# Kernel optimization log

Hardware: AMD Instinct MI355X
Metric: run time of the kernel (lower is better)

## Reference

```python
import jax, jax.numpy as jnp
import numpy as np

TEMPERATURE = 1.0


def setup_inputs() -> dict:
    key = jax.random.key(0)
    kq, kk, kv = jax.random.split(key, 3)
    shape = (2, 16, 2048, 64)  # B, H, L, D
    q = jax.random.normal(kq, shape, dtype=jnp.float32)
    k = jax.random.normal(kk, shape, dtype=jnp.float32)
    v = jax.random.normal(kv, shape, dtype=jnp.float32)
    return {"q": q, "k": k, "v": v}


def reference(q, k, v):
    # q, k, v: [B, H, L, D]
    L = q.shape[2]
    # scores: [B, H, L, L]; note: divided by temperature, NOT sqrt(D), per source
    scores = jnp.einsum("bhqd,bhkd->bhqk", q, k) / TEMPERATURE
    # causal mask: position j > i masked with -inf
    causal = jnp.tril(jnp.ones((L, L), dtype=bool))  # True = keep
    scores = jnp.where(causal, scores, -jnp.inf)
    attn = jax.nn.softmax(scores, axis=-1)
    out = jnp.einsum("bhqk,bhkd->bhqd", attn, v)
    return out
```

## Files before the change

### kernel.cpp

```cpp
#include <hip/hip_runtime.h>
#include <math.h>


typedef __attribute__((ext_vector_type(8))) _Float16 f16x8;
typedef __attribute__((ext_vector_type(4))) _Float16 f16x4;
typedef __attribute__((ext_vector_type(4))) float f32x4;
typedef __attribute__((ext_vector_type(16))) float f32x16;
typedef unsigned short u16;
typedef unsigned int u32;
typedef __attribute__((ext_vector_type(8))) u16 u16x8;
typedef __attribute__((ext_vector_type(4))) u32 u32x4;

constexpr int Lq = 2048;
constexpr int Dd = 64;
constexpr int KT = 64;
constexpr int BH = 32;
constexpr float LOG2E = 1.44269504088896f;

#define SWZB(row, bcol) ((((row) * 128) + (bcol)) ^ (((row) & 7) << 4))

#define GLOAD_LDS16(g, l)                                                     \
  __builtin_amdgcn_global_load_lds(                                           \
      (const __attribute__((address_space(1))) void*)(g),                     \
      (__attribute__((address_space(3))) void*)(l), 16, 0, 0)

static __device__ __forceinline__ u16 f2h(float x) {
  return __builtin_bit_cast(u16, (_Float16)x);
}

static __device__ __forceinline__ float tmax16(const f32x16& v) {
  float a = fmaxf(v[0], v[1]), b = fmaxf(v[2], v[3]);
  float c = fmaxf(v[4], v[5]), d = fmaxf(v[6], v[7]);
  float e = fmaxf(v[8], v[9]), f = fmaxf(v[10], v[11]);
  float g = fmaxf(v[12], v[13]), h = fmaxf(v[14], v[15]);
  a = fmaxf(a, b); c = fmaxf(c, d); e = fmaxf(e, f); g = fmaxf(g, h);
  return fmaxf(fmaxf(a, c), fmaxf(e, g));
}
static __device__ __forceinline__ float tsum16(const f32x16& v) {
  float a = v[0] + v[1], b = v[2] + v[3], c = v[4] + v[5], d = v[6] + v[7];
  float e = v[8] + v[9], f = v[10] + v[11], g = v[12] + v[13], h = v[14] + v[15];
  a += b; c += d; e += f; g += h;
  return (a + c) + (e + g);
}

constexpr int PREP_KB = (BH * Lq * Dd) / (256 * 16);

__global__ __launch_bounds__(256)
void attn_prep(const float* __restrict__ K, const float* __restrict__ V,
               u16* __restrict__ Kh, u16* __restrict__ VTh) {
  const int b = blockIdx.x;
  const int tid = threadIdx.x;
  if (b < PREP_KB) {
    const size_t base = ((size_t)b * 256 + tid) * 16;
    const f32x4* src = reinterpret_cast<const f32x4*>(K + base);
    u16x8 o0, o1;
    #pragma unroll
    for (int i = 0; i < 2; ++i) {
      const f32x4 a = src[i];
      #pragma unroll
      for (int j = 0; j < 4; ++j) o0[i * 4 + j] = f2h(a[j]);
    }
    #pragma unroll
    for (int i = 0; i < 2; ++i) {
      const f32x4 a = src[2 + i];
      #pragma unroll
      for (int j = 0; j < 4; ++j) o1[i * 4 + j] = f2h(a[j]);
    }
    *reinterpret_cast<u16x8*>(Kh + base) = o0;
    *reinterpret_cast<u16x8*>(Kh + base + 8) = o1;
  } else {
    __shared__ u16 lt[64][66];
    const int vb = b - PREP_KB;
    const int h = vb >> 5, tt = vb & 31;
    const float* Vt = V + ((size_t)h * Lq + tt * 64) * Dd;
    const int r = tid & 63, dg = tid >> 6;
    #pragma unroll
    for (int i = 0; i < 4; ++i) {
      const f32x4 a = *reinterpret_cast<const f32x4*>(Vt + (size_t)r * Dd + dg * 16 + i * 4);
      #pragma unroll
      for (int j = 0; j < 2; ++j) {
        const unsigned two =
            (unsigned)f2h(a[2 * j]) | ((unsigned)f2h(a[2 * j + 1]) << 16);
        *reinterpret_cast<unsigned*>(&lt[r][dg * 16 + i * 4 + j * 2]) = two;
      }
    }
    __syncthreads();
    const int d = tid >> 2, kq = tid & 3;
    u16x8 w0, w1;
    #pragma unroll
    for (int j = 0; j < 8; ++j) w0[j] = lt[kq * 16 + j][d];
    #pragma unroll
    for (int j = 0; j < 8; ++j) w1[j] = lt[kq * 16 + 8 + j][d];
    u16* dst = VTh + ((size_t)h * Dd + d) * Lq + tt * 64 + kq * 16;
    *reinterpret_cast<u16x8*>(dst) = w0;
    *reinterpret_cast<u16x8*>(dst + 8) = w1;
  }
}

__global__ __launch_bounds__(128)
void attn_main(const float* __restrict__ Q, float* __restrict__ O,
               const u16* __restrict__ Kh, const u16* __restrict__ VTh) {
  __shared__ char ks[2][8192];
  __shared__ char vt2[2][8192];
  __shared__ float bc[2][32];

  const int tid  = threadIdx.x;
  const int lane = tid & 63;
  const int wv   = tid >> 6;
  const int l31  = lane & 31;
  const int hi   = lane >> 5;

  const int b = blockIdx.x;
  const int chunk = 31 - (b >> 5);
  const int h = b & 31;

  const float* Qb = Q + (size_t)h * Lq * Dd;
  float*       Ob = O + (size_t)h * Lq * Dd;
  const u16*   Kb = Kh + (size_t)h * Lq * Dd;
  const u16*   Vb = VTh + (size_t)h * Dd * Lq;

  const int T    = chunk + 1;
  const int qrow = chunk * 64 + wv * 32;

  f16x8 qf[4];
  #pragma unroll
  for (int kc = 0; kc < 4; ++kc) {
    const float* qp = Qb + (size_t)(qrow + l31) * Dd + kc * 16 + hi * 8;
    const f32x4 a = *reinterpret_cast<const f32x4*>(qp);
    const f32x4 c = *reinterpret_cast<const f32x4*>(qp + 4);
    f16x8 q8;
    #pragma unroll
    for (int e = 0; e < 4; ++e) {
      q8[e]     = (_Float16)(a[e] * LOG2E);
      q8[e + 4] = (_Float16)(c[e] * LOG2E);
    }
    qf[kc] = q8;
  }

  float m = -INFINITY, lsum = 0.f;
  f32x16 o0, o1;
  #pragma unroll
  for (int e = 0; e < 16; ++e) { o0[e] = 0.f; o1[e] = 0.f; }

  const int rr = lane >> 3;
  const int c0 = (lane & 7) ^ rr;

  #pragma unroll
  for (int it = 0; it < 4; ++it) {
    const int row = wv * 32 + it * 8 + rr;
    GLOAD_LDS16(Kb + (size_t)row * Dd + c0 * 8,
                &ks[0][wv * 4096 + it * 1024 + lane * 16]);
    GLOAD_LDS16(Vb + (size_t)row * Lq + c0 * 8,
                &vt2[0][wv * 4096 + it * 1024 + lane * 16]);
  }

  int cur = 0;
  #pragma unroll 1
  for (int t = 0; t < T; ++t) {
    __syncthreads();
    if (t + 1 < T) {
      #pragma unroll
      for (int it = 0; it < 4; ++it) {
        const int row = wv * 32 + it * 8 + rr;
        GLOAD_LDS16(Kb + (size_t)((t + 1) * KT + row) * Dd + c0 * 8,
                    &ks[cur ^ 1][wv * 4096 + it * 1024 + lane * 16]);
        GLOAD_LDS16(Vb + (size_t)row * Lq + (t + 1) * KT + c0 * 8,
                    &vt2[cur ^ 1][wv * 4096 + it * 1024 + lane * 16]);
      }
    }
    const char* kb = ks[cur];
    const char* vb = vt2[cur];
    const bool last  = (t == T - 1);
    const bool have1 = !(last && wv == 0);

    f32x16 st0, st1;
    #pragma unroll
    for (int e = 0; e < 16; ++e) { st0[e] = 0.f; st1[e] = 0.f; }
    __builtin_amdgcn_s_setprio(1);
    #pragma unroll
    for (int kc = 0; kc < 4; ++kc) {
      const f16x8 kf = *reinterpret_cast<const f16x8*>(
          kb + SWZB(l31, kc * 32 + hi * 16));
      st0 = __builtin_amdgcn_mfma_f32_32x32x16_f16(kf, qf[kc], st0, 0, 0, 0);
    }
    if (have1) {
      #pragma unroll
      for (int kc = 0; kc < 4; ++kc) {
        const f16x8 kf = *reinterpret_cast<const f16x8*>(
            kb + SWZB(32 + l31, kc * 32 + hi * 16));
        st1 = __builtin_amdgcn_mfma_f32_32x32x16_f16(kf, qf[kc], st1, 0, 0, 0);
      }
    }
    __builtin_amdgcn_s_setprio(0);

    if (last) {
      #pragma unroll
      for (int r = 0; r < 16; ++r) {
        const int crow = (r & 3) + 8 * (r >> 2) + 4 * hi;
        if (wv == 0) { if (crow > l31) st0[r] = -INFINITY; }
        else         { if (crow > l31) st1[r] = -INFINITY; }
      }
    }

    float pm = tmax16(st0);
    if (have1) pm = fmaxf(pm, tmax16(st1));
    pm = fmaxf(pm, __shfl_xor(pm, 32));

    if (__any(pm > m + 8.f * LOG2E)) {
      const float mn = fmaxf(m, pm);
      const float sc = exp2f(m - mn);
      m = mn;
      lsum *= sc;
      if (hi == 0) bc[wv][l31] = sc;
      const f32x4 s0 = *reinterpret_cast<const f32x4*>(&bc[wv][4 * hi]);
      const f32x4 s1 = *reinterpret_cast<const f32x4*>(&bc[wv][8 + 4 * hi]);
      const f32x4 s2 = *reinterpret_cast<const f32x4*>(&bc[wv][16 + 4 * hi]);
      const f32x4 s3 = *reinterpret_cast<const f32x4*>(&bc[wv][24 + 4 * hi]);
      #pragma unroll
      for (int r = 0; r < 16; ++r) {
        const float fac = (r < 4) ? s0[r & 3] : (r < 8) ? s1[r & 3]
                        : (r < 12) ? s2[r & 3] : s3[r & 3];
        o0[r] *= fac;
        o1[r] *= fac;
      }
    }

    #pragma unroll
    for (int r = 0; r < 16; ++r) st0[r] = exp2f(st0[r] - m);
    float rs = tsum16(st0);
    if (have1) {
      #pragma unroll
      for (int r = 0; r < 16; ++r) st1[r] = exp2f(st1[r] - m);
      rs += tsum16(st1);
    }
    rs += __shfl_xor(rs, 32);
    lsum += rs;

    #pragma unroll
    for (int ksub = 0; ksub < 2; ++ksub) {
      if (ksub == 1 && !have1) break;
      const f32x16& st = (ksub == 0) ? st0 : st1;
      #pragma unroll
      for (int ks2 = 0; ks2 < 2; ++ks2) {
        const u32 pe0 = __builtin_bit_cast(u32,
            __builtin_amdgcn_cvt_pkrtz(st[8 * ks2 + 0], st[8 * ks2 + 1]));
        const u32 pe1 = __builtin_bit_cast(u32,
            __builtin_amdgcn_cvt_pkrtz(st[8 * ks2 + 2], st[8 * ks2 + 3]));
        const u32 po0 = __builtin_bit_cast(u32,
            __builtin_amdgcn_cvt_pkrtz(st[8 * ks2 + 4], st[8 * ks2 + 5]));
        const u32 po1 = __builtin_bit_cast(u32,
            __builtin_amdgcn_cvt_pkrtz(st[8 * ks2 + 6], st[8 * ks2 + 7]));
        const u32 ss0 = __shfl_xor(hi ? pe0 : po0, 32);
        const u32 ss1 = __shfl_xor(hi ? pe1 : po1, 32);
        u32x4 w;
        w[0] = hi ? ss0 : pe0;
        w[1] = hi ? ss1 : pe1;
        w[2] = hi ? po0 : ss0;
        w[3] = hi ? po1 : ss1;
        const f16x8 pa = __builtin_bit_cast(f16x8, w);
        const int cb = ksub * 64 + ks2 * 32 + hi * 16;
        const f16x8 v0 = *reinterpret_cast<const f16x8*>(vb + SWZB(l31, cb));
        const f16x8 v1 = *reinterpret_cast<const f16x8*>(vb + SWZB(32 + l31, cb));
        __builtin_amdgcn_s_setprio(1);
        o0 = __builtin_amdgcn_mfma_f32_32x32x16_f16(pa, v0, o0, 0, 0, 0);
        o1 = __builtin_amdgcn_mfma_f32_32x32x16_f16(pa, v1, o1, 0, 0, 0);
        __builtin_amdgcn_s_setprio(0);
      }
    }
    cur ^= 1;
  }

  const float inv = 1.f / lsum;
  if (hi == 0) bc[wv][l31] = inv;
  const f32x4 i0 = *reinterpret_cast<const f32x4*>(&bc[wv][4 * hi]);
  const f32x4 i1 = *reinterpret_cast<const f32x4*>(&bc[wv][8 + 4 * hi]);
  const f32x4 i2 = *reinterpret_cast<const f32x4*>(&bc[wv][16 + 4 * hi]);
  const f32x4 i3 = *reinterpret_cast<const f32x4*>(&bc[wv][24 + 4 * hi]);
  #pragma unroll
  for (int r = 0; r < 16; ++r) {
    const int crow = (r & 3) + 8 * (r >> 2) + 4 * hi;
    const float fac = (r < 4) ? i0[r & 3] : (r < 8) ? i1[r & 3]
                    : (r < 12) ? i2[r & 3] : i3[r & 3];
    float* op = Ob + (size_t)(qrow + crow) * Dd + l31;
    op[0]  = o0[r] * fac;
    op[32] = o1[r] * fac;
  }
}

__global__ __launch_bounds__(256)
void causal_attn_fb(const float* __restrict__ Q, const float* __restrict__ K,
                    const float* __restrict__ V, float* __restrict__ O) {
  __shared__ char ks[2][KT * 128];
  __shared__ char vt[2][Dd * 128];
  __shared__ char pl[4][16 * 128];
  const int tid = threadIdx.x, lane = tid & 63, wv = tid >> 6;
  const int l15 = lane & 15, g = lane >> 4;
  const int kg = tid & 15, dq = tid >> 4;
  const int bh = blockIdx.x / 16, pr = blockIdx.x % 16;
  const size_t base = (size_t)bh * Lq * Dd;
  const float* Qb = Q + base; const float* Kb = K + base;
  const float* Vb = V + base; float* Ob = O + base;
  char* pw = pl[wv];
  #pragma unroll 1
  for (int phase = 0; phase < 2; ++phase) {
    const int chunk = (phase == 0) ? pr : (31 - pr);
    const int row0 = chunk * 64, T = chunk + 1, qrow = row0 + wv * 16;
    f16x8 qf[2];
    #pragma unroll
    for (int kk = 0; kk < 2; ++kk) {
      const float* qp = Qb + (size_t)(qrow + l15) * Dd + kk * 32 + g * 8;
      const f32x4 a = *reinterpret_cast<const f32x4*>(qp);
      const f32x4 b = *reinterpret_cast<const f32x4*>(qp + 4);
      f16x8 q8;
      #pragma unroll
      for (int i = 0; i < 4; ++i) { q8[i] = (_Float16)a[i]; q8[i+4] = (_Float16)b[i]; }
      qf[kk] = q8;
    }
    float m[4], lsum[4]; f32x4 o[4];
    #pragma unroll
    for (int r = 0; r < 4; ++r) { m[r] = -INFINITY; lsum[r] = 0.f; }
    #pragma unroll
    for (int nd = 0; nd < 4; ++nd) o[nd] = f32x4{0.f, 0.f, 0.f, 0.f};
    {
      f32x4 kreg[4], vreg[4];
      #pragma unroll
      for (int i = 0; i < 4; ++i) {
        const int c = tid + i * 256;
        kreg[i] = *reinterpret_cast<const f32x4*>(Kb + (size_t)(c >> 4) * Dd + (c & 15) * 4);
      }
      #pragma unroll
      for (int c = 0; c < 4; ++c)
        vreg[c] = *reinterpret_cast<const f32x4*>(Vb + (size_t)(kg * 4 + c) * Dd + dq * 4);
      __syncthreads();
      #pragma unroll
      for (int i = 0; i < 4; ++i) {
        const int c = tid + i * 256;
        f16x4 hh;
        #pragma unroll
        for (int jj = 0; jj < 4; ++jj) hh[jj] = (_Float16)kreg[i][jj];
        *reinterpret_cast<f16x4*>(ks[0] + SWZB(c >> 4, (c & 15) * 8)) = hh;
      }
      #pragma unroll
      for (int jj = 0; jj < 4; ++jj) {
        f16x4 hh;
        #pragma unroll
        for (int c = 0; c < 4; ++c) hh[c] = (_Float16)vreg[c][jj];
        *reinterpret_cast<f16x4*>(vt[0] + SWZB(dq * 4 + jj, kg * 8)) = hh;
      }
    }
    int cur = 0;
    #pragma unroll 1
    for (int t = 0; t < T; ++t) {
      __syncthreads();
      const char* kb = ks[cur]; const char* vb = vt[cur];
      f32x4 kreg[4], vreg[4];
      const bool pfn = (t + 1 < T);
      if (pfn) {
        const float* Kt = Kb + (size_t)(t + 1) * KT * Dd;
        const float* Vt = Vb + (size_t)(t + 1) * KT * Dd;
        #pragma unroll
        for (int i = 0; i < 4; ++i) {
          const int c = tid + i * 256;
          kreg[i] = *reinterpret_cast<const f32x4*>(Kt + (size_t)(c >> 4) * Dd + (c & 15) * 4);
        }
        #pragma unroll
        for (int c = 0; c < 4; ++c)
          vreg[c] = *reinterpret_cast<const f32x4*>(Vt + (size_t)(kg * 4 + c) * Dd + dq * 4);
      }
      f32x4 s[4];
      #pragma unroll
      for (int n = 0; n < 4; ++n) s[n] = f32x4{0.f, 0.f, 0.f, 0.f};
      #pragma unroll
      for (int kk = 0; kk < 2; ++kk) {
        #pragma unroll
        for (int n = 0; n < 4; ++n) {
          const f16x8 kf = *reinterpret_cast<const f16x8*>(kb + SWZB(n * 16 + l15, kk * 64 + g * 16));
          s[n] = __builtin_amdgcn_mfma_f32_16x16x32_f16(qf[kk], kf, s[n], 0, 0, 0);
        }
      }
      if (t == T - 1) {
        #pragma unroll
        for (int n = 0; n < 4; ++n) {
          const int key = t * KT + n * 16 + l15;
          #pragma unroll
          for (int r = 0; r < 4; ++r)
            if (key > qrow + 4 * g + r) s[n][r] = -INFINITY;
        }
      }
      float rmax[4], rsum[4], scale[4];
      #pragma unroll
      for (int r = 0; r < 4; ++r)
        rmax[r] = fmaxf(fmaxf(s[0][r], s[1][r]), fmaxf(s[2][r], s[3][r]));
      #pragma unroll
      for (int mk = 1; mk <= 8; mk <<= 1) {
        #pragma unroll
        for (int r = 0; r < 4; ++r) rmax[r] = fmaxf(rmax[r], __shfl_xor(rmax[r], mk));
      }
      #pragma unroll
      for (int r = 0; r < 4; ++r) {
        const float mn = fmaxf(m[r], rmax[r]);
        scale[r] = __expf(m[r] - mn); m[r] = mn;
      }
      #pragma unroll
      for (int n = 0; n < 4; ++n) {
        #pragma unroll
        for (int r = 0; r < 4; ++r) s[n][r] = __expf(s[n][r] - m[r]);
      }
      #pragma unroll
      for (int r = 0; r < 4; ++r) rsum[r] = (s[0][r] + s[1][r]) + (s[2][r] + s[3][r]);
      #pragma unroll
      for (int mk = 1; mk <= 8; mk <<= 1) {
        #pragma unroll
        for (int r = 0; r < 4; ++r) rsum[r] += __shfl_xor(rsum[r], mk);
      }
      #pragma unroll
      for (int r = 0; r < 4; ++r) lsum[r] = lsum[r] * scale[r] + rsum[r];
      #pragma unroll
      for (int nd = 0; nd < 4; ++nd) {
        #pragma unroll
        for (int r = 0; r < 4; ++r) o[nd][r] *= scale[r];
      }
      #pragma unroll
      for (int n = 0; n < 4; ++n) {
        #pragma unroll
        for (int r = 0; r < 4; ++r)
          *reinterpret_cast<_Float16*>(pw + SWZB(4 * g + r, (n * 16 + l15) * 2)) = (_Float16)s[n][r];
      }
      asm volatile("s_waitcnt lgkmcnt(0)" ::: "memory");
      __builtin_amdgcn_sched_barrier(0);
      #pragma unroll
      for (int kblk = 0; kblk < 2; ++kblk) {
        const f16x8 pf = *reinterpret_cast<const f16x8*>(pw + SWZB(l15, kblk * 64 + g * 16));
        #pragma unroll
        for (int nd = 0; nd < 4; ++nd) {
          const f16x8 vf = *reinterpret_cast<const f16x8*>(vb + SWZB(nd * 16 + l15, kblk * 64 + g * 16));
          o[nd] = __builtin_amdgcn_mfma_f32_16x16x32_f16(pf, vf, o[nd], 0, 0, 0);
        }
      }
      if (pfn) {
        char* kn = ks[cur ^ 1]; char* vn = vt[cur ^ 1];
        #pragma unroll
        for (int i = 0; i < 4; ++i) {
          const int c = tid + i * 256;
          f16x4 hh;
          #pragma unroll
          for (int jj = 0; jj < 4; ++jj) hh[jj] = (_Float16)kreg[i][jj];
          *reinterpret_cast<f16x4*>(kn + SWZB(c >> 4, (c & 15) * 8)) = hh;
        }
        #pragma unroll
        for (int jj = 0; jj < 4; ++jj) {
          f16x4 hh;
          #pragma unroll
          for (int c = 0; c < 4; ++c) hh[c] = (_Float16)vreg[c][jj];
          *reinterpret_cast<f16x4*>(vn + SWZB(dq * 4 + jj, kg * 8)) = hh;
        }
      }
      cur ^= 1;
    }
    float inv[4];
    #pragma unroll
    for (int r = 0; r < 4; ++r) inv[r] = 1.f / lsum[r];
    #pragma unroll
    for (int nd = 0; nd < 4; ++nd) {
      #pragma unroll
      for (int r = 0; r < 4; ++r)
        Ob[(size_t)(qrow + 4 * g + r) * Dd + nd * 16 + l15] = o[nd][r] * inv[r];
    }
  }
}

extern "C" void kernel_launch(void* const* d_in, const int* in_sizes, int n_in,
                              void* d_out, int out_size, void* d_ws, size_t ws_size,
                              hipStream_t stream) {
  const float* q = (const float*)d_in[0];
  const float* k = (const float*)d_in[1];
  const float* v = (const float*)d_in[2];
  float* o = (float*)d_out;
  const size_t elems = (size_t)BH * Lq * Dd;
  const size_t need = elems * 2 * 2;
  if (ws_size >= need) {
    u16* Kh = (u16*)d_ws;
    u16* VTh = Kh + elems;
    attn_prep<<<dim3(2 * PREP_KB), dim3(256), 0, stream>>>(k, v, Kh, VTh);
    attn_main<<<dim3(BH * 32), dim3(128), 0, stream>>>(q, o, Kh, VTh);
  } else {
    causal_attn_fb<<<dim3(BH * 16), dim3(256), 0, stream>>>(q, k, v, o);
  }
  (void)in_sizes; (void)n_in; (void)out_size;
}
```

Before: 84.43 us.

## Use single-wave blocks with 32-row query and key tiles, dropping block barriers

Each attention block now has one 64-lane wave and handles 32 query rows, with 32-key tiles, launching twice as many blocks. Because the block is a single wave, __syncthreads is replaced by explicit vmcnt waits on the async global-to-LDS prefetches. V tiles use a new 64-byte-row swizzle. This aims for finer-grained causal load balance, more resident blocks and no cross-wave barriers, at the cost of twice the loop iterations per row, more per-tile overhead and each block reloading K/V independently, which doubles K/V traffic.

```diff
diff --git a/kernel.cpp b/kernel.cpp
--- a/kernel.cpp
+++ b/kernel.cpp
@@ -18,6 +18,7 @@
 constexpr float LOG2E = 1.44269504088896f;
 
 #define SWZB(row, bcol) ((((row) * 128) + (bcol)) ^ (((row) & 7) << 4))
+#define SWZB64(row, bcol) ((((row) * 64) + (bcol)) ^ ((((row) >> 1) & 3) << 4))
 
 #define GLOAD_LDS16(g, l)                                                     \
   __builtin_amdgcn_global_load_lds(                                           \
@@ -97,21 +98,19 @@
   }
 }
 
-__global__ __launch_bounds__(128)
+__global__ __launch_bounds__(64)
 void attn_main(const float* __restrict__ Q, float* __restrict__ O,
                const u16* __restrict__ Kh, const u16* __restrict__ VTh) {
-  __shared__ char ks[2][8192];
-  __shared__ char vt2[2][8192];
-  __shared__ float bc[2][32];
-
-  const int tid  = threadIdx.x;
-  const int lane = tid & 63;
-  const int wv   = tid >> 6;
+  __shared__ char ksA[2][4096];
+  __shared__ char vtA[2][4096];
+  __shared__ float bc[32];
+
+  const int lane = threadIdx.x;
   const int l31  = lane & 31;
   const int hi   = lane >> 5;
 
   const int b = blockIdx.x;
-  const int chunk = 31 - (b >> 5);
+  const int chunk = 63 - (b >> 5);
   const int h = b & 31;
 
   const float* Qb = Q + (size_t)h * Lq * Dd;
@@ -120,7 +119,7 @@
   const u16*   Vb = VTh + (size_t)h * Dd * Lq;
 
   const int T    = chunk + 1;
-  const int qrow = chunk * 64 + wv * 32;
+  const int qrow = chunk * 32;
 
   f16x8 qf[4];
   #pragma unroll
@@ -142,40 +141,46 @@
   #pragma unroll
   for (int e = 0; e < 16; ++e) { o0[e] = 0.f; o1[e] = 0.f; }
 
-  const int rr = lane >> 3;
-  const int c0 = (lane & 7) ^ rr;
-
-  #pragma unroll
-  for (int it = 0; it < 4; ++it) {
-    const int row = wv * 32 + it * 8 + rr;
-    GLOAD_LDS16(Kb + (size_t)row * Dd + c0 * 8,
-                &ks[0][wv * 4096 + it * 1024 + lane * 16]);
-    GLOAD_LDS16(Vb + (size_t)row * Lq + c0 * 8,
-                &vt2[0][wv * 4096 + it * 1024 + lane * 16]);
-  }
+  const int rrK = lane >> 3;
+  const int c0K = (lane & 7) ^ (rrK & 7);
+  const int rrV = lane >> 2;
+  const int c0V = (lane & 3) ^ ((lane >> 3) & 3);
+
+#define STAGE(t_, buf_)                                                       \
+  do {                                                                        \
+    const u16* Kt_ = Kb + (size_t)(t_) * 32 * Dd;                             \
+    _Pragma("unroll")                                                         \
+    for (int it = 0; it < 4; ++it) {                                          \
+      GLOAD_LDS16(Kt_ + (size_t)(it * 8 + rrK) * Dd + c0K * 8,                \
+                  &ksA[buf_][it * 1024 + lane * 16]);                         \
+    }                                                                         \
+    _Pragma("unroll")                                                         \
+    for (int it = 0; it < 4; ++it) {                                          \
+      GLOAD_LDS16(Vb + (size_t)(it * 16 + rrV) * Lq + (t_) * 32 + c0V * 8,    \
+                  &vtA[buf_][it * 1024 + lane * 16]);                         \
+    }                                                                         \
+  } while (0)
+
+  STAGE(0, 0);
 
   int cur = 0;
   #pragma unroll 1
   for (int t = 0; t < T; ++t) {
-    __syncthreads();
-    if (t + 1 < T) {
-      #pragma unroll
-      for (int it = 0; it < 4; ++it) {
-        const int row = wv * 32 + it * 8 + rr;
-        GLOAD_LDS16(Kb + (size_t)((t + 1) * KT + row) * Dd + c0 * 8,
-                    &ks[cur ^ 1][wv * 4096 + it * 1024 + lane * 16]);
-        GLOAD_LDS16(Vb + (size_t)row * Lq + (t + 1) * KT + c0 * 8,
-                    &vt2[cur ^ 1][wv * 4096 + it * 1024 + lane * 16]);
-      }
-    }
-    const char* kb = ks[cur];
-    const char* vb = vt2[cur];
-    const bool last  = (t == T - 1);
-    const bool have1 = !(last && wv == 0);
-
-    f32x16 st0, st1;
-    #pragma unroll
-    for (int e = 0; e < 16; ++e) { st0[e] = 0.f; st1[e] = 0.f; }
+    const bool pf = (t + 1 < T);
+    if (pf) {
+      STAGE(t + 1, cur ^ 1);
+      asm volatile("s_waitcnt vmcnt(8)" ::: "memory");
+    } else {
+      asm volatile("s_waitcnt vmcnt(0)" ::: "memory");
+    }
+    __builtin_amdgcn_sched_barrier(0);
+    const char* kb = ksA[cur];
+    const char* vb = vtA[cur];
+    const bool last = (t == T - 1);
+
+    f32x16 st0;
+    #pragma unroll
+    for (int e = 0; e < 16; ++e) st0[e] = 0.f;
     __builtin_amdgcn_s_setprio(1);
     #pragma unroll
     for (int kc = 0; kc < 4; ++kc) {
@@ -183,27 +188,17 @@
           kb + SWZB(l31, kc * 32 + hi * 16));
       st0 = __builtin_amdgcn_mfma_f32_32x32x16_f16(kf, qf[kc], st0, 0, 0, 0);
     }
-    if (have1) {
-      #pragma unroll
-      for (int kc = 0; kc < 4; ++kc) {
-        const f16x8 kf = *reinterpret_cast<const f16x8*>(
-            kb + SWZB(32 + l31, kc * 32 + hi * 16));
-        st1 = __builtin_amdgcn_mfma_f32_32x32x16_f16(kf, qf[kc], st1, 0, 0, 0);
-      }
-    }
     __builtin_amdgcn_s_setprio(0);
 
     if (last) {
       #pragma unroll
       for (int r = 0; r < 16; ++r) {
         const int crow = (r & 3) + 8 * (r >> 2) + 4 * hi;
-        if (wv == 0) { if (crow > l31) st0[r] = -INFINITY; }
-        else         { if (crow > l31) st1[r] = -INFINITY; }
+        if (crow > l31) st0[r] = -INFINITY;
       }
     }
 
     float pm = tmax16(st0);
-    if (have1) pm = fmaxf(pm, tmax16(st1));
     pm = fmaxf(pm, __shfl_xor(pm, 32));
 
     if (__any(pm > m + 8.f * LOG2E)) {
@@ -211,11 +206,11 @@
       const float sc = exp2f(m - mn);
       m = mn;
       lsum *= sc;
-      if (hi == 0) bc[wv][l31] = sc;
-      const f32x4 s0 = *reinterpret_cast<const f32x4*>(&bc[wv][4 * hi]);
-      const f32x4 s1 = *reinterpret_cast<const f32x4*>(&bc[wv][8 + 4 * hi]);
-      const f32x4 s2 = *reinterpret_cast<const f32x4*>(&bc[wv][16 + 4 * hi]);
-      const f32x4 s3 = *reinterpret_cast<const f32x4*>(&bc[wv][24 + 4 * hi]);
+      if (hi == 0) bc[l31] = sc;
+      const f32x4 s0 = *reinterpret_cast<const f32x4*>(&bc[4 * hi]);
+      const f32x4 s1 = *reinterpret_cast<const f32x4*>(&bc[8 + 4 * hi]);
+      const f32x4 s2 = *reinterpret_cast<const f32x4*>(&bc[16 + 4 * hi]);
+      const f32x4 s3 = *reinterpret_cast<const f32x4*>(&bc[24 + 4 * hi]);
       #pragma unroll
       for (int r = 0; r < 16; ++r) {
         const float fac = (r < 4) ? s0[r & 3] : (r < 8) ? s1[r & 3]
@@ -228,54 +223,44 @@
     #pragma unroll
     for (int r = 0; r < 16; ++r) st0[r] = exp2f(st0[r] - m);
     float rs = tsum16(st0);
-    if (have1) {
-      #pragma unroll
-      for (int r = 0; r < 16; ++r) st1[r] = exp2f(st1[r] - m);
-      rs += tsum16(st1);
-    }
     rs += __shfl_xor(rs, 32);
     lsum += rs;
 
     #pragma unroll
-    for (int ksub = 0; ksub < 2; ++ksub) {
-      if (ksub == 1 && !have1) break;
-      const f32x16& st = (ksub == 0) ? st0 : st1;
-      #pragma unroll
-      for (int ks2 = 0; ks2 < 2; ++ks2) {
-        const u32 pe0 = __builtin_bit_cast(u32,
-            __builtin_amdgcn_cvt_pkrtz(st[8 * ks2 + 0], st[8 * ks2 + 1]));
-        const u32 pe1 = __builtin_bit_cast(u32,
-            __builtin_amdgcn_cvt_pkrtz(st[8 * ks2 + 2], st[8 * ks2 + 3]));
-        const u32 po0 = __builtin_bit_cast(u32,
-            __builtin_amdgcn_cvt_pkrtz(st[8 * ks2 + 4], st[8 * ks2 + 5]));
-        const u32 po1 = __builtin_bit_cast(u32,
-            __builtin_amdgcn_cvt_pkrtz(st[8 * ks2 + 6], st[8 * ks2 + 7]));
-        const u32 ss0 = __shfl_xor(hi ? pe0 : po0, 32);
-        const u32 ss1 = __shfl_xor(hi ? pe1 : po1, 32);
-        u32x4 w;
-        w[0] = hi ? ss0 : pe0;
-        w[1] = hi ? ss1 : pe1;
-        w[2] = hi ? po0 : ss0;
-        w[3] = hi ? po1 : ss1;
-        const f16x8 pa = __builtin_bit_cast(f16x8, w);
-        const int cb = ksub * 64 + ks2 * 32 + hi * 16;
-        const f16x8 v0 = *reinterpret_cast<const f16x8*>(vb + SWZB(l31, cb));
-        const f16x8 v1 = *reinterpret_cast<const f16x8*>(vb + SWZB(32 + l31, cb));
-        __builtin_amdgcn_s_setprio(1);
-        o0 = __builtin_amdgcn_mfma_f32_32x32x16_f16(pa, v0, o0, 0, 0, 0);
-        o1 = __builtin_amdgcn_mfma_f32_32x32x16_f16(pa, v1, o1, 0, 0, 0);
-        __builtin_amdgcn_s_setprio(0);
-      }
+    for (int ks2 = 0; ks2 < 2; ++ks2) {
+      const u32 pe0 = __builtin_bit_cast(u32,
+          __builtin_amdgcn_cvt_pkrtz(st0[8 * ks2 + 0], st0[8 * ks2 + 1]));
+      const u32 pe1 = __builtin_bit_cast(u32,
+          __builtin_amdgcn_cvt_pkrtz(st0[8 * ks2 + 2], st0[8 * ks2 + 3]));
+      const u32 po0 = __builtin_bit_cast(u32,
+          __builtin_amdgcn_cvt_pkrtz(st0[8 * ks2 + 4], st0[8 * ks2 + 5]));
+      const u32 po1 = __builtin_bit_cast(u32,
+          __builtin_amdgcn_cvt_pkrtz(st0[8 * ks2 + 6], st0[8 * ks2 + 7]));
+      const u32 ss0 = __shfl_xor(hi ? pe0 : po0, 32);
+      const u32 ss1 = __shfl_xor(hi ? pe1 : po1, 32);
+      u32x4 w;
+      w[0] = hi ? ss0 : pe0;
+      w[1] = hi ? ss1 : pe1;
+      w[2] = hi ? po0 : ss0;
+      w[3] = hi ? po1 : ss1;
+      const f16x8 pa = __builtin_bit_cast(f16x8, w);
+      const int cb = ks2 * 32 + hi * 16;
+      const f16x8 v0 = *reinterpret_cast<const f16x8*>(vb + SWZB64(l31, cb));
+      const f16x8 v1 = *reinterpret_cast<const f16x8*>(vb + SWZB64(32 + l31, cb));
+      __builtin_amdgcn_s_setprio(1);
+      o0 = __builtin_amdgcn_mfma_f32_32x32x16_f16(pa, v0, o0, 0, 0, 0);
+      o1 = __builtin_amdgcn_mfma_f32_32x32x16_f16(pa, v1, o1, 0, 0, 0);
+      __builtin_amdgcn_s_setprio(0);
     }
     cur ^= 1;
   }
 
   const float inv = 1.f / lsum;
-  if (hi == 0) bc[wv][l31] = inv;
-  const f32x4 i0 = *reinterpret_cast<const f32x4*>(&bc[wv][4 * hi]);
-  const f32x4 i1 = *reinterpret_cast<const f32x4*>(&bc[wv][8 + 4 * hi]);
-  const f32x4 i2 = *reinterpret_cast<const f32x4*>(&bc[wv][16 + 4 * hi]);
-  const f32x4 i3 = *reinterpret_cast<const f32x4*>(&bc[wv][24 + 4 * hi]);
+  if (hi == 0) bc[l31] = inv;
+  const f32x4 i0 = *reinterpret_cast<const f32x4*>(&bc[4 * hi]);
+  const f32x4 i1 = *reinterpret_cast<const f32x4*>(&bc[8 + 4 * hi]);
+  const f32x4 i2 = *reinterpret_cast<const f32x4*>(&bc[16 + 4 * hi]);
+  const f32x4 i3 = *reinterpret_cast<const f32x4*>(&bc[24 + 4 * hi]);
   #pragma unroll
   for (int r = 0; r < 16; ++r) {
     const int crow = (r & 3) + 8 * (r >> 2) + 4 * hi;
@@ -285,6 +270,7 @@
     op[0]  = o0[r] * fac;
     op[32] = o1[r] * fac;
   }
+#undef STAGE
 }
 
 __global__ __launch_bounds__(256)
@@ -482,7 +468,7 @@
     u16* Kh = (u16*)d_ws;
     u16* VTh = Kh + elems;
     attn_prep<<<dim3(2 * PREP_KB), dim3(256), 0, stream>>>(k, v, Kh, VTh);
-    attn_main<<<dim3(BH * 32), dim3(128), 0, stream>>>(q, o, Kh, VTh);
+    attn_main<<<dim3(BH * 64), dim3(64), 0, stream>>>(q, o, Kh, VTh);
   } else {
     causal_attn_fb<<<dim3(BH * 16), dim3(256), 0, stream>>>(q, k, v, o);
   }
```

Measured after the change: 94.64 us. 12.1% more time.
